# Kernel optimization log

Hardware: AMD Instinct MI355X
Metric: run time of the kernel (lower is better)

## Reference

```python
import jax, jax.numpy as jnp
import numpy as np

N, M, E, F, OUT = 20000, 2048, 320000, 512, 2
HID = F // 2
NEG_ATT = 0.2   # leaky_relu slope inside HypergraphConv attention
NEG = 0.01      # default F.leaky_relu / nn.LeakyReLU slope
EPS = 1e-5      # GraphNorm eps


def setup_inputs() -> dict:
    key = jax.random.key(0)
    ks = jax.random.split(key, 12)
    nrm = lambda k, shape, s=0.05: (jax.random.normal(k, shape, jnp.float32) * s)
    row = jax.random.randint(ks[1], (E,), 0, N)
    col = jax.random.randint(ks[2], (E,), 0, M)
    return dict(
        x=nrm(ks[0], (N, F), 1.0),
        edge_index=jnp.stack([row, col]),                 # [2, E] int32
        edge_attr=nrm(ks[3], (M, F), 1.0),
        W1=nrm(ks[4], (F, F)), att1=nrm(ks[5], (2 * F,)), b1=jnp.zeros((F,), jnp.float32),
        W2=nrm(ks[6], (F, F)), att2=nrm(ks[7], (2 * F,)), b2=jnp.zeros((F,), jnp.float32),
        gn1_w=jnp.ones((F,), jnp.float32), gn1_b=jnp.zeros((F,), jnp.float32), gn1_ms=jnp.ones((F,), jnp.float32),
        gn2_w=jnp.ones((F,), jnp.float32), gn2_b=jnp.zeros((F,), jnp.float32), gn2_ms=jnp.ones((F,), jnp.float32),
        fc1_W=nrm(ks[8], (F, HID)), fc1_b=jnp.zeros((HID,), jnp.float32),
        fc2_W=nrm(ks[9], (F, HID)), fc2_b=jnp.zeros((HID,), jnp.float32),
        cls_W=nrm(ks[10], (HID, OUT)), cls_b=jnp.zeros((OUT,), jnp.float32),
    )


def _segsum(v, idx, n):
    return jax.ops.segment_sum(v, idx, num_segments=n)


def hypergraph_conv(x, edge_attr, row, col, W, att, bias):
    """PyG HypergraphConv, heads=1, use_attention=True, attention_mode='node'."""
    xl = x @ W                          # [N, F] node features after lin
    el = edge_attr @ W                  # [M, F] hyperedge features after lin
    # attention logits per incidence: (cat[x_i, e_j] * att).sum(-1)
    pre = xl[row] @ att[:F] + el[col] @ att[F:]           # [E]
    alpha = jax.nn.leaky_relu(pre, NEG_ATT)
    # softmax grouped by hyperedge (col)
    amax = jax.ops.segment_max(alpha, col, num_segments=M)
    amax = jnp.where(jnp.isfinite(amax), amax, 0.0)
    ex = jnp.exp(alpha - amax[col])
    denom = _segsum(ex, col, M)
    alpha = ex / jnp.maximum(denom, 1e-16)[col]           # [E]
    # degree normalizations (hyperedge_weight = 1)
    ones = jnp.ones((row.shape[0],), xl.dtype)
    deg_n = _segsum(ones, row, N)
    Dinv = jnp.where(deg_n > 0, 1.0 / deg_n, 0.0)         # [N]
    deg_e = _segsum(ones, col, M)
    Binv = jnp.where(deg_e > 0, 1.0 / deg_e, 0.0)         # [M]
    # propagate 1: nodes -> hyperedges
    edge_feat = _segsum((alpha * Binv[col])[:, None] * xl[row], col, M)   # [M, F]
    # propagate 2: hyperedges -> nodes
    out = _segsum((alpha * Dinv[row])[:, None] * edge_feat[col], row, N)  # [N, F]
    return out + bias


def graph_norm(x, w, b, ms):
    # single graph (batch=None): normalize over all nodes
    mean = x.mean(axis=0)
    out = x - ms * mean
    var = (out * out).mean(axis=0)
    return out / jnp.sqrt(var + EPS) * w + b


def reference(x, edge_index, edge_attr,
              W1, att1, b1, W2, att2, b2,
              gn1_w, gn1_b, gn1_ms, gn2_w, gn2_b, gn2_ms,
              fc1_W, fc1_b, fc2_W, fc2_b, cls_W, cls_b):
    row, col = edge_index[0], edge_index[1]
    h = hypergraph_conv(x, edge_attr, row, col, W1, att1, b1)
    h = jax.nn.leaky_relu(graph_norm(h, gn1_w, gn1_b, gn1_ms), NEG)
    out = jax.nn.leaky_relu(h @ fc1_W + fc1_b, NEG)
    h = hypergraph_conv(h, edge_attr, row, col, W2, att2, b2)
    h = jax.nn.leaky_relu(graph_norm(h, gn2_w, gn2_b, gn2_ms), NEG)
    out = out + jax.nn.leaky_relu(h @ fc2_W + fc2_b, NEG)
    logits = out @ cls_W + cls_b
    return logits
```

## Files before the change

### kernel.cpp

```cpp
#include <hip/hip_runtime.h>
#include <math.h>

#define FDIM 512
#define HIDDIM 256
#define HB 128
#define SCH 1024
#define LDSK 32

typedef __bf16 bf16x8 __attribute__((ext_vector_type(8)));
typedef float floatx4 __attribute__((ext_vector_type(4)));

__device__ __forceinline__ float lrelu(float x, float s) { return x >= 0.0f ? x : s * x; }

__device__ __forceinline__ float bf2f(unsigned int u) {
  union { float f; unsigned int i; } v; v.i = u << 16; return v.f;
}
__device__ __forceinline__ unsigned short f2bf(float f) {
  union { float f; unsigned int u; } v; v.f = f;
  unsigned int x = v.u;
  return (unsigned short)((x + 0x7fffu + ((x >> 16) & 1u)) >> 16);
}

__device__ __forceinline__ void async_copy16(const unsigned short* g, unsigned short* l) {
  __builtin_amdgcn_global_load_lds((const __attribute__((address_space(1))) unsigned int*)g,
                                   (__attribute__((address_space(3))) unsigned int*)l, 16, 0, 0);
}

__device__ __forceinline__ float waveReduceSum(float v) {
#pragma unroll
  for (int o = 32; o; o >>= 1) v += __shfl_down(v, o, 64);
  return v;
}

__device__ __forceinline__ float blockReduceSum256(float v) {
  __shared__ float sm[4];
  int lane = threadIdx.x & 63, w = threadIdx.x >> 6;
  v = waveReduceSum(v);
  __syncthreads();
  if (lane == 0) sm[w] = v;
  __syncthreads();
  return sm[0] + sm[1] + sm[2] + sm[3];
}

__device__ __forceinline__ float blockReduceMax256(float v) {
  __shared__ float sm[4];
  int lane = threadIdx.x & 63, w = threadIdx.x >> 6;
#pragma unroll
  for (int o = 32; o; o >>= 1) v = fmaxf(v, __shfl_down(v, o, 64));
  __syncthreads();
  if (lane == 0) sm[w] = v;
  __syncthreads();
  return fmaxf(fmaxf(sm[0], sm[1]), fmaxf(sm[2], sm[3]));
}

__global__ __launch_bounds__(256) void k_hist2(const int* __restrict__ row, const int* __restrict__ col,
                                               int* __restrict__ cnt_r, int* __restrict__ cnt_c,
                                               int E, int nchunk) {
  __shared__ int h[2048];
  int b = blockIdx.x, t = threadIdx.x;
  for (int i = t; i < 2048; i += 256) h[i] = 0;
  __syncthreads();
  int s = b * nchunk, e = min(E, s + nchunk);
  for (int j = s + t; j < e; j += 256) {
    atomicAdd(&h[col[j]], 1);
    atomicAdd(&cnt_r[row[j]], 1);
  }
  __syncthreads();
  for (int i = t; i < 2048; i += 256) {
    int v = h[i];
    if (v) atomicAdd(&cnt_c[i], v);
  }
}

__global__ __launch_bounds__(256) void k_scan_part(const int* __restrict__ cnt, int* __restrict__ off,
                                                   int* __restrict__ btot, int n) {
  int b = blockIdx.x, t = threadIdx.x;
  int base = b * SCH + t * 4;
  int v[4];
#pragma unroll
  for (int i = 0; i < 4; ++i) v[i] = (base + i < n) ? cnt[base + i] : 0;
  int s = v[0] + v[1] + v[2] + v[3];
  int lane = t & 63, w = t >> 6;
  int x = s;
#pragma unroll
  for (int o = 1; o < 64; o <<= 1) {
    int y = __shfl_up(x, o, 64);
    if (lane >= o) x += y;
  }
  __shared__ int ws[4];
  if (lane == 63) ws[w] = x;
  __syncthreads();
  int wpre = 0;
  for (int i = 0; i < w; ++i) wpre += ws[i];
  int run = wpre + x - s;
#pragma unroll
  for (int i = 0; i < 4; ++i) {
    if (base + i < n) off[base + i] = run;
    run += v[i];
  }
  if (t == 255) btot[b] = wpre + x;
}

__global__ __launch_bounds__(256) void k_scan_midcol(int* __restrict__ btot, int nb,
                                                     const int* __restrict__ cnt_c, int* __restrict__ off_c,
                                                     int* __restrict__ gcur) {
  int t = threadIdx.x, lane = t & 63, w = t >> 6;
  __shared__ int ws[4];
  if (blockIdx.x == 0) {
    int v = (t < nb) ? btot[t] : 0;
    int x = v;
#pragma unroll
    for (int o = 1; o < 64; o <<= 1) {
      int y = __shfl_up(x, o, 64);
      if (lane >= o) x += y;
    }
    if (lane == 63) ws[w] = x;
    __syncthreads();
    int wpre = 0;
    for (int i = 0; i < w; ++i) wpre += ws[i];
    if (t < nb) btot[t] = wpre + x - v;
    if (t == 255) btot[nb] = wpre + x;
  } else {
    int base = t * 8;
    int v[8];
#pragma unroll
    for (int i = 0; i < 8; ++i) v[i] = cnt_c[base + i];
    int s = 0;
#pragma unroll
    for (int i = 0; i < 8; ++i) s += v[i];
    int x = s;
#pragma unroll
    for (int o = 1; o < 64; o <<= 1) {
      int y = __shfl_up(x, o, 64);
      if (lane >= o) x += y;
    }
    if (lane == 63) ws[w] = x;
    __syncthreads();
    int wpre = 0;
    for (int i = 0; i < w; ++i) wpre += ws[i];
    int run = wpre + x - s;
#pragma unroll
    for (int i = 0; i < 8; ++i) {
      off_c[base + i] = run;
      gcur[base + i] = run;
      run += v[i];
    }
    if (t == 255) off_c[2048] = wpre + x;
  }
}

__global__ __launch_bounds__(256) void k_scan_add(int* __restrict__ off, const int* __restrict__ btot,
                                                  int n, int nb) {
  int b = blockIdx.x, t = threadIdx.x;
  int base = b * SCH + t * 4;
  int add = btot[b];
#pragma unroll
  for (int i = 0; i < 4; ++i)
    if (base + i < n) off[base + i] += add;
  if (b == 0 && t == 0) off[n] = btot[nb];
}

__global__ __launch_bounds__(256) void k_fill3(const int* __restrict__ row, const int* __restrict__ col,
                                               int* __restrict__ gcur, const int* __restrict__ off_r,
                                               int* __restrict__ cur_r, int* __restrict__ csr_c,
                                               int* __restrict__ rj, int* __restrict__ cj,
                                               int* __restrict__ pos_r, int E, int nchunk) {
  __shared__ int h[2048];
  __shared__ int lbase[2048];
  int b = blockIdx.x, t = threadIdx.x;
  for (int i = t; i < 2048; i += 256) h[i] = 0;
  __syncthreads();
  int s = b * nchunk, e = min(E, s + nchunk);
  for (int j = s + t; j < e; j += 256) atomicAdd(&h[col[j]], 1);
  __syncthreads();
  for (int i = t; i < 2048; i += 256) {
    int c = h[i];
    lbase[i] = c ? atomicAdd(&gcur[i], c) : 0;
    h[i] = 0;
  }
  __syncthreads();
  for (int j = s + t; j < e; j += 256) {
    int r = row[j], c = col[j];
    int slot_c = lbase[c] + atomicAdd(&h[c], 1);
    csr_c[slot_c] = j;
    rj[slot_c] = r;
    int slot_r = off_r[r] + atomicAdd(&cur_r[r], 1);
    cj[slot_r] = c;
    pos_r[j] = slot_r;
  }
}

__global__ __launch_bounds__(256) void k_hi(const float* __restrict__ A, unsigned short* __restrict__ hi, int n4) {
  int i = blockIdx.x * 256 + threadIdx.x;
  if (i < n4) {
    float4 v = ((const float4*)A)[i];
    ushort4 h;
    h.x = f2bf(v.x); h.y = f2bf(v.y); h.z = f2bf(v.z); h.w = f2bf(v.w);
    ((ushort4*)hi)[i] = h;
  }
}

__global__ __launch_bounds__(256) void k_prep_w_hi2(const float* __restrict__ W1, unsigned short* __restrict__ t1,
                                                    const float* __restrict__ W2, unsigned short* __restrict__ t2,
                                                    int K, int Nc) {
  const float* W = blockIdx.z ? W2 : W1;
  unsigned short* th = blockIdx.z ? t2 : t1;
  int n = blockIdx.x * 16 + (threadIdx.x & 15);
  int k = blockIdx.y * 16 + (threadIdx.x >> 4);
  th[(size_t)n * K + k] = f2bf(W[(size_t)k * Nc + n]);
}

__global__ __launch_bounds__(256) void k_prep_w2(const float* __restrict__ Wa, unsigned short* __restrict__ tha,
                                                 unsigned short* __restrict__ tla, const float* __restrict__ Wb,
                                                 unsigned short* __restrict__ thb, unsigned short* __restrict__ tlb,
                                                 int K, int Nc) {
  const float* W = blockIdx.z ? Wb : Wa;
  unsigned short* th = blockIdx.z ? thb : tha;
  unsigned short* tl = blockIdx.z ? tlb : tla;
  int n = blockIdx.x * 16 + (threadIdx.x & 15);
  int k = blockIdx.y * 16 + (threadIdx.x >> 4);
  float v = W[(size_t)k * Nc + n];
  unsigned short h = f2bf(v);
  unsigned short l = f2bf(v - bf2f(h));
  th[(size_t)n * K + k] = h;
  tl[(size_t)n * K + k] = l;
}

__global__ __launch_bounds__(256) void k_wv2(const float* __restrict__ W1, const float* __restrict__ a1,
                                             const float* __restrict__ W2, const float* __restrict__ a2,
                                             float* __restrict__ wv1, float* __restrict__ wv2) {
  int lane = threadIdx.x & 63, w = threadIdx.x >> 6;
  int k = blockIdx.x * 4 + w;
  const float* W = blockIdx.y ? W2 : W1;
  const float* a = blockIdx.y ? a2 : a1;
  float* wv = blockIdx.y ? wv2 : wv1;
  float s = 0.f;
  for (int f = lane; f < FDIM; f += 64) s = fmaf(W[(size_t)k * FDIM + f], a[f], s);
  s = waveReduceSum(s);
  if (lane == 0) wv[k] = s;
}

__global__ __launch_bounds__(256) void k_ea2(const float* __restrict__ X, const float* __restrict__ wv1,
                                             const float* __restrict__ wv2, float* __restrict__ ea1,
                                             float* __restrict__ ea2, int Mr) {
  int lane = threadIdx.x & 63, w = threadIdx.x >> 6;
  int m = blockIdx.x * 4 + w;
  if (m < Mr) {
    float s1 = 0.f, s2 = 0.f;
    for (int f = lane; f < FDIM; f += 64) {
      float v = X[(size_t)m * FDIM + f];
      s1 = fmaf(v, wv1[f], s1);
      s2 = fmaf(v, wv2[f], s2);
    }
    s1 = waveReduceSum(s1);
    s2 = waveReduceSum(s2);
    if (lane == 0) { ea1[m] = s1; ea2[m] = s2; }
  }
}

__global__ __launch_bounds__(256, 1) void gemm_conv(const unsigned short* __restrict__ Ah,
                                                    const unsigned short* __restrict__ Bth,
                                                    unsigned short* __restrict__ Cb,
                                                    const float* __restrict__ att, float* __restrict__ xa,
                                                    int Mr, int K, int Nc) {
  __shared__ unsigned short lds[2 * 128 * LDSK];
  int tid = threadIdx.x, lane = tid & 63, w = tid >> 6;
  int wr = w >> 1, wc = w & 1;
  int rowB = blockIdx.y * 128, colB = blockIdx.x * 128;

  const unsigned short* src = (w < 2) ? Ah : Bth;
  int baseRow = ((w < 2) ? rowB : colB) + 64 * (w & 1);
  int maxRow = (w < 2) ? (Mr - 1) : (Nc - 1);
  int slr = lane >> 2, slc = lane & 3;
  unsigned short* dstBase = &lds[((w >> 1) * 128 + (w & 1) * 64) * LDSK];

  size_t gro[4];
#pragma unroll
  for (int seg = 0; seg < 4; ++seg) {
    int rg = baseRow + seg * 16 + slr;
    if (rg > maxRow) rg = maxRow;
    gro[seg] = (size_t)rg * K + slc * 8;
  }

  floatx4 zero4 = {0.f, 0.f, 0.f, 0.f};
  floatx4 acc[4][4];
#pragma unroll
  for (int i = 0; i < 4; ++i)
#pragma unroll
    for (int j = 0; j < 4; ++j) acc[i][j] = zero4;

  int fr = lane & 15, fq = lane >> 4;
  int offA = (wr * 64 + fr) * LDSK + fq * 8;
  int offB = 128 * LDSK + (wc * 64 + fr) * LDSK + fq * 8;

  for (int k0 = 0; k0 < K; k0 += 32) {
#pragma unroll
    for (int seg = 0; seg < 4; ++seg) async_copy16(src + gro[seg] + k0, dstBase + seg * 16 * LDSK);
    __syncthreads();
    bf16x8 a[4], b[4];
#pragma unroll
    for (int t = 0; t < 4; ++t) {
      a[t] = *(const bf16x8*)(&lds[offA + t * 16 * LDSK]);
      b[t] = *(const bf16x8*)(&lds[offB + t * 16 * LDSK]);
    }
#pragma unroll
    for (int ti = 0; ti < 4; ++ti)
#pragma unroll
      for (int tj = 0; tj < 4; ++tj)
        acc[ti][tj] = __builtin_amdgcn_mfma_f32_16x16x32_bf16(a[ti], b[tj], acc[ti][tj], 0, 0, 0);
    __syncthreads();
  }

  int colL = colB + wc * 64 + fr;
  int rowL = rowB + wr * 64 + fq * 4;
  float attv[4];
#pragma unroll
  for (int tj = 0; tj < 4; ++tj) attv[tj] = att[colL + tj * 16];
#pragma unroll
  for (int ti = 0; ti < 4; ++ti) {
#pragma unroll
    for (int r = 0; r < 4; ++r) {
      int rr = rowL + ti * 16 + r;
      if (rr < Mr) {
        float dot = 0.f;
#pragma unroll
        for (int tj = 0; tj < 4; ++tj) {
          float v = acc[ti][tj][r];
          Cb[(size_t)rr * Nc + colL + tj * 16] = f2bf(v);
          dot = fmaf(v, attv[tj], dot);
        }
#pragma unroll
        for (int o = 1; o < 16; o <<= 1) dot += __shfl_xor(dot, o, 64);
        if ((lane & 15) == 0) atomicAdd(&xa[rr], dot);
      }
    }
  }
}

template <int EPI>
__global__ __launch_bounds__(256, 1) void gemm_fc(const unsigned short* __restrict__ Ahi,
                                                  const unsigned short* __restrict__ Bthi,
                                                  const unsigned short* __restrict__ Btlo,
                                                  float* __restrict__ Cf, const float* __restrict__ bias,
                                                  int Mr, int K, int Nc) {
  __shared__ unsigned short lds[3 * 128 * LDSK];
  int tid = threadIdx.x, lane = tid & 63, w = tid >> 6;
  int wr = w >> 1, wc = w & 1;
  int rowB = blockIdx.y * 128, colB = blockIdx.x * 128;

  const unsigned short* src;
  int baseRow, maxRow, nseg;
  unsigned short* dstBase;
  if (w < 2) { src = Ahi; baseRow = rowB + 64 * w; maxRow = Mr - 1; nseg = 4; dstBase = &lds[w * 64 * LDSK]; }
  else if (w == 2) { src = Bthi; baseRow = colB; maxRow = Nc - 1; nseg = 8; dstBase = &lds[128 * LDSK]; }
  else { src = Btlo; baseRow = colB; maxRow = Nc - 1; nseg = 8; dstBase = &lds[2 * 128 * LDSK]; }

  int slr = lane >> 2, slc = lane & 3;
  size_t gro[8];
  for (int seg = 0; seg < nseg; ++seg) {
    int rg = baseRow + seg * 16 + slr;
    if (rg > maxRow) rg = maxRow;
    gro[seg] = (size_t)rg * K + slc * 8;
  }

  floatx4 zero4 = {0.f, 0.f, 0.f, 0.f};
  floatx4 acc[4][4];
#pragma unroll
  for (int i = 0; i < 4; ++i)
#pragma unroll
    for (int j = 0; j < 4; ++j) acc[i][j] = zero4;

  int fr = lane & 15, fq = lane >> 4;
  int offA = (wr * 64 + fr) * LDSK + fq * 8;
  int offBh = 128 * LDSK + (wc * 64 + fr) * LDSK + fq * 8;

  for (int k0 = 0; k0 < K; k0 += 32) {
    for (int seg = 0; seg < nseg; ++seg) async_copy16(src + gro[seg] + k0, dstBase + seg * 16 * LDSK);
    __syncthreads();
    bf16x8 a[4], bh[4], bl[4];
#pragma unroll
    for (int t = 0; t < 4; ++t) {
      a[t] = *(const bf16x8*)(&lds[offA + t * 16 * LDSK]);
      bh[t] = *(const bf16x8*)(&lds[offBh + t * 16 * LDSK]);
      bl[t] = *(const bf16x8*)(&lds[128 * LDSK + offBh + t * 16 * LDSK]);
    }
#pragma unroll
    for (int ti = 0; ti < 4; ++ti)
#pragma unroll
      for (int tj = 0; tj < 4; ++tj) {
        acc[ti][tj] = __builtin_amdgcn_mfma_f32_16x16x32_bf16(a[ti], bh[tj], acc[ti][tj], 0, 0, 0);
        acc[ti][tj] = __builtin_amdgcn_mfma_f32_16x16x32_bf16(a[ti], bl[tj], acc[ti][tj], 0, 0, 0);
      }
    __syncthreads();
  }

  int colL = colB + wc * 64 + fr;
  int rowL = rowB + wr * 64 + fq * 4;
#pragma unroll
  for (int tj = 0; tj < 4; ++tj) {
    int c = colL + tj * 16;
    float bb = bias[c];
#pragma unroll
    for (int ti = 0; ti < 4; ++ti) {
#pragma unroll
      for (int r = 0; r < 4; ++r) {
        int rr = rowL + ti * 16 + r;
        if (rr < Mr) {
          float v = lrelu(acc[ti][tj][r] + bb, 0.01f);
          if (EPI == 1) Cf[(size_t)rr * Nc + c] = v;
          else Cf[(size_t)rr * Nc + c] += v;
        }
      }
    }
  }
}

__global__ __launch_bounds__(256) void k_prop_col_f(const unsigned short* __restrict__ xl,
                                                    const float* __restrict__ xa, const float* __restrict__ ea,
                                                    const int* __restrict__ rj, const int* __restrict__ csr_c,
                                                    const int* __restrict__ pos_r, const int* __restrict__ off_c,
                                                    float* __restrict__ arj, unsigned short* __restrict__ ef) {
  int m = blockIdx.x;
  int s = off_c[m], e_ = off_c[m + 1];
  int cnt = e_ - s;
  float eam = ea[m];
  int t = threadIdx.x, lane = t & 63, w = t >> 6;

  float mx = -3.402823466e38f;
  for (int j = s + t; j < e_; j += 256) mx = fmaxf(mx, lrelu(xa[rj[j]] + eam, 0.2f));
  mx = blockReduceMax256(mx);
  float sum = 0.f;
  for (int j = s + t; j < e_; j += 256) sum += expf(lrelu(xa[rj[j]] + eam, 0.2f) - mx);
  sum = blockReduceSum256(sum);
  float inv = 1.0f / fmaxf(sum, 1e-16f);

  __shared__ int sidx[512];
  __shared__ float swgt[512];
  __shared__ float pf[4][512];
  float acc[8] = {0, 0, 0, 0, 0, 0, 0, 0};
  for (int base = 0; base < cnt; base += 512) {
    int n = min(512, cnt - base);
    for (int j = t; j < n; j += 256) {
      int g = s + base + j;
      int r = rj[g];
      float a = expf(lrelu(xa[r] + eam, 0.2f) - mx) * inv;
      sidx[j] = r;
      swgt[j] = a;
      arj[pos_r[csr_c[g]]] = a;
    }
    __syncthreads();
    int j = w;
    for (; j + 16 <= n; j += 16) {
      int r0 = sidx[j], r1 = sidx[j + 4], r2 = sidx[j + 8], r3 = sidx[j + 12];
      float w0 = swgt[j], w1 = swgt[j + 4], w2 = swgt[j + 8], w3 = swgt[j + 12];
      bf16x8 v0 = *(const bf16x8*)(xl + (size_t)r0 * FDIM + lane * 8);
      bf16x8 v1 = *(const bf16x8*)(xl + (size_t)r1 * FDIM + lane * 8);
      bf16x8 v2 = *(const bf16x8*)(xl + (size_t)r2 * FDIM + lane * 8);
      bf16x8 v3 = *(const bf16x8*)(xl + (size_t)r3 * FDIM + lane * 8);
#pragma unroll
      for (int i = 0; i < 8; ++i) acc[i] = fmaf(w0, (float)v0[i], acc[i]);
#pragma unroll
      for (int i = 0; i < 8; ++i) acc[i] = fmaf(w1, (float)v1[i], acc[i]);
#pragma unroll
      for (int i = 0; i < 8; ++i) acc[i] = fmaf(w2, (float)v2[i], acc[i]);
#pragma unroll
      for (int i = 0; i < 8; ++i) acc[i] = fmaf(w3, (float)v3[i], acc[i]);
    }
    for (; j < n; j += 4) {
      int r = sidx[j];
      float wt = swgt[j];
      bf16x8 v = *(const bf16x8*)(xl + (size_t)r * FDIM + lane * 8);
#pragma unroll
      for (int i = 0; i < 8; ++i) acc[i] = fmaf(wt, (float)v[i], acc[i]);
    }
    __syncthreads();
  }
  float binv = cnt > 0 ? 1.0f / (float)cnt : 0.0f;
#pragma unroll
  for (int i = 0; i < 8; i += 2) *(float2*)&pf[w][lane * 8 + i] = make_float2(acc[i] * binv, acc[i + 1] * binv);
  __syncthreads();
  float2 r0 = ((const float2*)pf[0])[t], r1 = ((const float2*)pf[1])[t];
  float2 r2 = ((const float2*)pf[2])[t], r3 = ((const float2*)pf[3])[t];
  float a0 = r0.x + r1.x + r2.x + r3.x;
  float a1 = r0.y + r1.y + r2.y + r3.y;
  unsigned int o = (unsigned int)f2bf(a0) | ((unsigned int)f2bf(a1) << 16);
  ((unsigned int*)(ef + (size_t)m * FDIM))[t] = o;
}

__global__ __launch_bounds__(256) void k_prop_row(const unsigned short* __restrict__ ef,
                                                  const float* __restrict__ arj, const int* __restrict__ cj,
                                                  const int* __restrict__ off_r, const float* __restrict__ bias,
                                                  unsigned short* __restrict__ hb) {
  int nB = blockIdx.x;
  int s = off_r[nB], e_ = off_r[nB + 1];
  int cnt = e_ - s;
  __shared__ int sidx[512];
  __shared__ float swgt[512];
  __shared__ float pf[4][512];
  int t = threadIdx.x, lane = t & 63, w = t >> 6;
  float acc[8] = {0, 0, 0, 0, 0, 0, 0, 0};
  for (int base = 0; base < cnt; base += 512) {
    int n = min(512, cnt - base);
    for (int j = t; j < n; j += 256) {
      sidx[j] = cj[s + base + j];
      swgt[j] = arj[s + base + j];
    }
    __syncthreads();
    int j = w;
    for (; j + 8 <= n; j += 8) {
      int r0 = sidx[j], r1 = sidx[j + 4];
      float w0 = swgt[j], w1 = swgt[j + 4];
      bf16x8 v0 = *(const bf16x8*)(ef + (size_t)r0 * FDIM + lane * 8);
      bf16x8 v1 = *(const bf16x8*)(ef + (size_t)r1 * FDIM + lane * 8);
#pragma unroll
      for (int i = 0; i < 8; ++i) acc[i] = fmaf(w0, (float)v0[i], acc[i]);
#pragma unroll
      for (int i = 0; i < 8; ++i) acc[i] = fmaf(w1, (float)v1[i], acc[i]);
    }
    for (; j < n; j += 4) {
      int r = sidx[j];
      float wt = swgt[j];
      bf16x8 v = *(const bf16x8*)(ef + (size_t)r * FDIM + lane * 8);
#pragma unroll
      for (int i = 0; i < 8; ++i) acc[i] = fmaf(wt, (float)v[i], acc[i]);
    }
    __syncthreads();
  }
  float dinv = cnt > 0 ? 1.0f / (float)cnt : 0.0f;
#pragma unroll
  for (int i = 0; i < 8; i += 2) *(float2*)&pf[w][lane * 8 + i] = make_float2(acc[i] * dinv, acc[i + 1] * dinv);
  __syncthreads();
  float2 r0 = ((const float2*)pf[0])[t], r1 = ((const float2*)pf[1])[t];
  float2 r2 = ((const float2*)pf[2])[t], r3 = ((const float2*)pf[3])[t];
  float a0 = r0.x + r1.x + r2.x + r3.x + bias[2 * t];
  float a1 = r0.y + r1.y + r2.y + r3.y + bias[2 * t + 1];
  unsigned int o = (unsigned int)f2bf(a0) | ((unsigned int)f2bf(a1) << 16);
  ((unsigned int*)(hb + (size_t)nB * FDIM))[t] = o;
}

__global__ __launch_bounds__(256) void k_stats(const unsigned short* __restrict__ hb, float* __restrict__ gsum,
                                               float* __restrict__ gsq, int N) {
  int t = threadIdx.x;
  float s0 = 0, q0 = 0, s1 = 0, q1 = 0;
  for (int r = blockIdx.x; r < N; r += gridDim.x) {
    unsigned int u = ((const unsigned int*)(hb + (size_t)r * FDIM))[t];
    float v0 = bf2f(u & 0xffffu), v1 = bf2f(u >> 16);
    s0 += v0; q0 = fmaf(v0, v0, q0);
    s1 += v1; q1 = fmaf(v1, v1, q1);
  }
  atomicAdd(&gsum[2 * t], s0);
  atomicAdd(&gsq[2 * t], q0);
  atomicAdd(&gsum[2 * t + 1], s1);
  atomicAdd(&gsq[2 * t + 1], q1);
}

__global__ __launch_bounds__(256) void k_napply(const unsigned short* __restrict__ hb,
                                                const float* __restrict__ gsum, const float* __restrict__ gsq,
                                                const float* __restrict__ ms, const float* __restrict__ wg,
                                                const float* __restrict__ b, unsigned short* __restrict__ hi,
                                                float invn, int total2) {
  int i = blockIdx.x * 256 + threadIdx.x;
  if (i < total2) {
    int f2 = i & 255;
    int f0 = 2 * f2, f1 = 2 * f2 + 1;
    float mean0 = gsum[f0] * invn, mean1 = gsum[f1] * invn;
    float m0 = ms[f0], m1 = ms[f1];
    float var0 = gsq[f0] * invn - (2.0f * m0 - m0 * m0) * mean0 * mean0;
    float var1 = gsq[f1] * invn - (2.0f * m1 - m1 * m1) * mean1 * mean1;
    float scl0 = wg[f0] * __frsqrt_rn(var0 + 1e-5f);
    float scl1 = wg[f1] * __frsqrt_rn(var1 + 1e-5f);
    unsigned int u = ((const unsigned int*)hb)[i];
    float v0 = bf2f(u & 0xffffu), v1 = bf2f(u >> 16);
    v0 = lrelu((v0 - m0 * mean0) * scl0 + b[f0], 0.01f);
    v1 = lrelu((v1 - m1 * mean1) * scl1 + b[f1], 0.01f);
    ((unsigned int*)hi)[i] = (unsigned int)f2bf(v0) | ((unsigned int)f2bf(v1) << 16);
  }
}

__global__ __launch_bounds__(256) void k_cls(const float* __restrict__ out1, const float* __restrict__ W,
                                             const float* __restrict__ b, float* __restrict__ logits, int N) {
  __shared__ float Ws[512];
  int t = threadIdx.x;
  Ws[t] = W[t];
  Ws[256 + t] = W[256 + t];
  __syncthreads();
  int lane = t & 63, w = t >> 6;
  int r = blockIdx.x * 4 + w;
  if (r < N) {
    float a0 = 0.f, a1 = 0.f;
    for (int k = lane; k < 256; k += 64) {
      float v = out1[(size_t)r * 256 + k];
      a0 = fmaf(v, Ws[2 * k], a0);
      a1 = fmaf(v, Ws[2 * k + 1], a1);
    }
#pragma unroll
    for (int o = 32; o; o >>= 1) {
      a0 += __shfl_down(a0, o, 64);
      a1 += __shfl_down(a1, o, 64);
    }
    if (lane == 0) {
      logits[(size_t)r * 2] = a0 + b[0];
      logits[(size_t)r * 2 + 1] = a1 + b[1];
    }
  }
}

extern "C" void kernel_launch(void* const* d_in, const int* in_sizes, int n_in,
                              void* d_out, int out_size, void* d_ws, size_t ws_size,
                              hipStream_t stream) {
  const float* x      = (const float*)d_in[0];
  const int*   eidx   = (const int*)d_in[1];
  const float* eattr  = (const float*)d_in[2];
  const float* W1     = (const float*)d_in[3];
  const float* att1   = (const float*)d_in[4];
  const float* b1     = (const float*)d_in[5];
  const float* W2     = (const float*)d_in[6];
  const float* att2   = (const float*)d_in[7];
  const float* b2     = (const float*)d_in[8];
  const float* gn1_w  = (const float*)d_in[9];
  const float* gn1_b  = (const float*)d_in[10];
  const float* gn1_ms = (const float*)d_in[11];
  const float* gn2_w  = (const float*)d_in[12];
  const float* gn2_b  = (const float*)d_in[13];
  const float* gn2_ms = (const float*)d_in[14];
  const float* fc1_W  = (const float*)d_in[15];
  const float* fc1_b  = (const float*)d_in[16];
  const float* fc2_W  = (const float*)d_in[17];
  const float* fc2_b  = (const float*)d_in[18];
  const float* cls_W  = (const float*)d_in[19];
  const float* cls_b  = (const float*)d_in[20];
  float* logits = (float*)d_out;

  const int N = in_sizes[0] / FDIM;
  const int E = in_sizes[1] / 2;
  const int M = in_sizes[2] / FDIM;
  const int* row = eidx;
  const int* col = eidx + E;
  const size_t NS = (size_t)N * FDIM;
  const size_t MS = (size_t)M * FDIM;

  char* base = (char*)d_ws;
  auto alloc = [&](size_t bytes) { char* r = base; base += (bytes + 255) & ~(size_t)255; return r; };

  unsigned short* xhi = (unsigned short*)alloc(NS * 2);
  unsigned short* xl  = (unsigned short*)alloc(NS * 2);
  unsigned short* hb  = (unsigned short*)alloc(NS * 2);
  unsigned short* ef  = (unsigned short*)alloc(MS * 2);
  float* out1 = (float*)alloc((size_t)N * HIDDIM * 4);
  unsigned short* w1th = (unsigned short*)alloc(FDIM * FDIM * 2);
  unsigned short* w2th = (unsigned short*)alloc(FDIM * FDIM * 2);
  unsigned short* f1th = (unsigned short*)alloc(FDIM * HIDDIM * 2);
  unsigned short* f1tl = (unsigned short*)alloc(FDIM * HIDDIM * 2);
  unsigned short* f2th = (unsigned short*)alloc(FDIM * HIDDIM * 2);
  unsigned short* f2tl = (unsigned short*)alloc(FDIM * HIDDIM * 2);
  float* wv1 = (float*)alloc(FDIM * 4);
  float* wv2 = (float*)alloc(FDIM * 4);
  float* ea1 = (float*)alloc((size_t)M * 4);
  float* ea2 = (float*)alloc((size_t)M * 4);
  float* arj = (float*)alloc((size_t)E * 4);
  int* off_r = (int*)alloc((size_t)(N + 1) * 4);
  int* off_c = (int*)alloc((size_t)(M + 1) * 4);
  int* gcur  = (int*)alloc((size_t)M * 4);
  int* csr_c = (int*)alloc((size_t)E * 4);
  int* rj    = (int*)alloc((size_t)E * 4);
  int* cj    = (int*)alloc((size_t)E * 4);
  int* pos_r = (int*)alloc((size_t)E * 4);
  int* btot  = (int*)alloc(512 * 4);

  char* zstart = base;
  int* cnt_r = (int*)alloc((size_t)(2 * N + M) * 4);
  int* cur_r = cnt_r + N;
  int* cnt_c = cur_r + N;
  float* xa1 = (float*)alloc((size_t)N * 4);
  float* xa2 = (float*)alloc((size_t)N * 4);
  float* gsum1 = (float*)alloc(FDIM * 4);
  float* gsq1  = (float*)alloc(FDIM * 4);
  float* gsum2 = (float*)alloc(FDIM * 4);
  float* gsq2  = (float*)alloc(FDIM * 4);
  size_t zlen = (size_t)(base - zstart);
  hipMemsetAsync(zstart, 0, zlen, stream);

  int nchunk = (E + HB - 1) / HB;
  int nbR = (N + SCH - 1) / SCH;
  k_hist2<<<HB, 256, 0, stream>>>(row, col, cnt_r, cnt_c, E, nchunk);
  k_scan_part<<<nbR, 256, 0, stream>>>(cnt_r, off_r, btot, N);
  k_scan_midcol<<<2, 256, 0, stream>>>(btot, nbR, cnt_c, off_c, gcur);
  k_scan_add<<<nbR, 256, 0, stream>>>(off_r, btot, N, nbR);
  k_fill3<<<HB, 256, 0, stream>>>(row, col, gcur, off_r, cur_r, csr_c, rj, cj, pos_r, E, nchunk);

  k_hi<<<(int)((NS / 4 + 255) / 256), 256, 0, stream>>>(x, xhi, (int)(NS / 4));
  k_prep_w_hi2<<<dim3(FDIM / 16, FDIM / 16, 2), 256, 0, stream>>>(W1, w1th, W2, w2th, FDIM, FDIM);
  k_prep_w2<<<dim3(HIDDIM / 16, FDIM / 16, 2), 256, 0, stream>>>(fc1_W, f1th, f1tl, fc2_W, f2th, f2tl, FDIM, HIDDIM);
  k_wv2<<<dim3(FDIM / 4, 2), 256, 0, stream>>>(W1, att1 + FDIM, W2, att2 + FDIM, wv1, wv2);
  k_ea2<<<(M + 3) / 4, 256, 0, stream>>>(eattr, wv1, wv2, ea1, ea2, M);

  int gN128 = (N + 127) / 128;
  int napply_grid = (int)((NS / 2 + 255) / 256);
  float invn = 1.0f / (float)N;

  gemm_conv<<<dim3(FDIM / 128, gN128), 256, 0, stream>>>(xhi, w1th, xl, att1, xa1, N, FDIM, FDIM);
  k_prop_col_f<<<M, 256, 0, stream>>>(xl, xa1, ea1, rj, csr_c, pos_r, off_c, arj, ef);
  k_prop_row<<<N, 256, 0, stream>>>(ef, arj, cj, off_r, b1, hb);
  k_stats<<<256, 256, 0, stream>>>(hb, gsum1, gsq1, N);
  k_napply<<<napply_grid, 256, 0, stream>>>(hb, gsum1, gsq1, gn1_ms, gn1_w, gn1_b, xhi, invn, (int)(NS / 2));
  gemm_fc<1><<<dim3(HIDDIM / 128, gN128), 256, 0, stream>>>(xhi, f1th, f1tl, out1, fc1_b, N, FDIM, HIDDIM);

  gemm_conv<<<dim3(FDIM / 128, gN128), 256, 0, stream>>>(xhi, w2th, xl, att2, xa2, N, FDIM, FDIM);
  k_prop_col_f<<<M, 256, 0, stream>>>(xl, xa2, ea2, rj, csr_c, pos_r, off_c, arj, ef);
  k_prop_row<<<N, 256, 0, stream>>>(ef, arj, cj, off_r, b2, hb);
  k_stats<<<256, 256, 0, stream>>>(hb, gsum2, gsq2, N);
  k_napply<<<napply_grid, 256, 0, stream>>>(hb, gsum2, gsq2, gn2_ms, gn2_w, gn2_b, xhi, invn, (int)(NS / 2));
  gemm_fc<2><<<dim3(HIDDIM / 128, gN128), 256, 0, stream>>>(xhi, f2th, f2tl, out1, fc2_b, N, FDIM, HIDDIM);

  k_cls<<<(N + 3) / 4, 256, 0, stream>>>(out1, cls_W, cls_b, logits, N);
}
```

Before: 579.5 us.

## Fuse both FC GEMMs with classifier and cache softmax logits in LDS

Merges the two fc GEMMs and the classifier into one kernel. Each block computes both fc tiles for a 64-column slice, applies bias and leaky-relu, and atomically adds its partial logits, so the fp32 out1 buffer and the separate k_cls pass go away. The normalized activations of each layer now go to separate buffers. Hyperedge softmax now stores logits in LDS when degree is at most 512, avoiding repeated gathers of xa. The csr_c/pos_r double indirection becomes a single prj array. The trade-offs are more atomics on logits, nondeterministic summation order, and two extra activation buffers.

```diff
diff --git a/kernel.cpp b/kernel.cpp
--- a/kernel.cpp
+++ b/kernel.cpp
@@ -162,9 +162,9 @@
 
 __global__ __launch_bounds__(256) void k_fill3(const int* __restrict__ row, const int* __restrict__ col,
                                                int* __restrict__ gcur, const int* __restrict__ off_r,
-                                               int* __restrict__ cur_r, int* __restrict__ csr_c,
+                                               int* __restrict__ cur_r, int* __restrict__ prj,
                                                int* __restrict__ rj, int* __restrict__ cj,
-                                               int* __restrict__ pos_r, int E, int nchunk) {
+                                               int E, int nchunk) {
   __shared__ int h[2048];
   __shared__ int lbase[2048];
   int b = blockIdx.x, t = threadIdx.x;
@@ -182,11 +182,10 @@
   for (int j = s + t; j < e; j += 256) {
     int r = row[j], c = col[j];
     int slot_c = lbase[c] + atomicAdd(&h[c], 1);
-    csr_c[slot_c] = j;
+    int slot_r = off_r[r] + atomicAdd(&cur_r[r], 1);
     rj[slot_c] = r;
-    int slot_r = off_r[r] + atomicAdd(&cur_r[r], 1);
+    prj[slot_c] = slot_r;
     cj[slot_r] = c;
-    pos_r[j] = slot_r;
   }
 }
 
@@ -337,78 +336,120 @@
   }
 }
 
-template <int EPI>
-__global__ __launch_bounds__(256, 1) void gemm_fc(const unsigned short* __restrict__ Ahi,
-                                                  const unsigned short* __restrict__ Bthi,
-                                                  const unsigned short* __restrict__ Btlo,
-                                                  float* __restrict__ Cf, const float* __restrict__ bias,
-                                                  int Mr, int K, int Nc) {
-  __shared__ unsigned short lds[3 * 128 * LDSK];
+__global__ __launch_bounds__(256, 1) void gemm_fc_cls(const unsigned short* __restrict__ A1,
+                                                      const unsigned short* __restrict__ B1h,
+                                                      const unsigned short* __restrict__ B1l,
+                                                      const float* __restrict__ b1,
+                                                      const unsigned short* __restrict__ A2,
+                                                      const unsigned short* __restrict__ B2h,
+                                                      const unsigned short* __restrict__ B2l,
+                                                      const float* __restrict__ b2,
+                                                      const float* __restrict__ clsW, const float* __restrict__ clsb,
+                                                      float* __restrict__ logits, int Mr, int K) {
+  __shared__ unsigned short lds[(128 + 2 * 64) * LDSK];
   int tid = threadIdx.x, lane = tid & 63, w = tid >> 6;
   int wr = w >> 1, wc = w & 1;
-  int rowB = blockIdx.y * 128, colB = blockIdx.x * 128;
-
-  const unsigned short* src;
-  int baseRow, maxRow, nseg;
-  unsigned short* dstBase;
-  if (w < 2) { src = Ahi; baseRow = rowB + 64 * w; maxRow = Mr - 1; nseg = 4; dstBase = &lds[w * 64 * LDSK]; }
-  else if (w == 2) { src = Bthi; baseRow = colB; maxRow = Nc - 1; nseg = 8; dstBase = &lds[128 * LDSK]; }
-  else { src = Btlo; baseRow = colB; maxRow = Nc - 1; nseg = 8; dstBase = &lds[2 * 128 * LDSK]; }
+  int rowB = blockIdx.y * 128, colB = blockIdx.x * 64;
 
   int slr = lane >> 2, slc = lane & 3;
-  size_t gro[8];
-  for (int seg = 0; seg < nseg; ++seg) {
+  int baseRow = (w < 2) ? (rowB + 64 * w) : colB;
+  int maxRow = (w < 2) ? (Mr - 1) : (HIDDIM - 1);
+  unsigned short* dstBase = &lds[w * 64 * LDSK];
+
+  size_t gro[4];
+#pragma unroll
+  for (int seg = 0; seg < 4; ++seg) {
     int rg = baseRow + seg * 16 + slr;
     if (rg > maxRow) rg = maxRow;
     gro[seg] = (size_t)rg * K + slc * 8;
   }
 
-  floatx4 zero4 = {0.f, 0.f, 0.f, 0.f};
-  floatx4 acc[4][4];
-#pragma unroll
-  for (int i = 0; i < 4; ++i)
-#pragma unroll
-    for (int j = 0; j < 4; ++j) acc[i][j] = zero4;
-
   int fr = lane & 15, fq = lane >> 4;
   int offA = (wr * 64 + fr) * LDSK + fq * 8;
-  int offBh = 128 * LDSK + (wc * 64 + fr) * LDSK + fq * 8;
-
-  for (int k0 = 0; k0 < K; k0 += 32) {
-    for (int seg = 0; seg < nseg; ++seg) async_copy16(src + gro[seg] + k0, dstBase + seg * 16 * LDSK);
-    __syncthreads();
-    bf16x8 a[4], bh[4], bl[4];
-#pragma unroll
-    for (int t = 0; t < 4; ++t) {
-      a[t] = *(const bf16x8*)(&lds[offA + t * 16 * LDSK]);
-      bh[t] = *(const bf16x8*)(&lds[offBh + t * 16 * LDSK]);
-      bl[t] = *(const bf16x8*)(&lds[128 * LDSK + offBh + t * 16 * LDSK]);
-    }
-#pragma unroll
-    for (int ti = 0; ti < 4; ++ti)
-#pragma unroll
-      for (int tj = 0; tj < 4; ++tj) {
-        acc[ti][tj] = __builtin_amdgcn_mfma_f32_16x16x32_bf16(a[ti], bh[tj], acc[ti][tj], 0, 0, 0);
-        acc[ti][tj] = __builtin_amdgcn_mfma_f32_16x16x32_bf16(a[ti], bl[tj], acc[ti][tj], 0, 0, 0);
+  int offBh = (128 + wc * 32 + fr) * LDSK + fq * 8;
+  int offBl = offBh + 64 * LDSK;
+
+  floatx4 zero4 = {0.f, 0.f, 0.f, 0.f};
+  floatx4 acc1[4][2], acc2[4][2];
+#pragma unroll
+  for (int i = 0; i < 4; ++i) {
+    acc1[i][0] = zero4; acc1[i][1] = zero4;
+    acc2[i][0] = zero4; acc2[i][1] = zero4;
+  }
+
+#pragma unroll
+  for (int L = 0; L < 2; ++L) {
+    const unsigned short* src =
+        (L == 0) ? ((w < 2) ? A1 : (w == 2) ? B1h : B1l)
+                 : ((w < 2) ? A2 : (w == 2) ? B2h : B2l);
+    for (int k0 = 0; k0 < K; k0 += 32) {
+#pragma unroll
+      for (int seg = 0; seg < 4; ++seg) async_copy16(src + gro[seg] + k0, dstBase + seg * 16 * LDSK);
+      __syncthreads();
+      bf16x8 a[4], bh[2], bl[2];
+#pragma unroll
+      for (int t = 0; t < 4; ++t) a[t] = *(const bf16x8*)(&lds[offA + t * 16 * LDSK]);
+#pragma unroll
+      for (int t = 0; t < 2; ++t) {
+        bh[t] = *(const bf16x8*)(&lds[offBh + t * 16 * LDSK]);
+        bl[t] = *(const bf16x8*)(&lds[offBl + t * 16 * LDSK]);
       }
-    __syncthreads();
-  }
-
-  int colL = colB + wc * 64 + fr;
+      if (L == 0) {
+#pragma unroll
+        for (int ti = 0; ti < 4; ++ti)
+#pragma unroll
+          for (int tj = 0; tj < 2; ++tj) {
+            acc1[ti][tj] = __builtin_amdgcn_mfma_f32_16x16x32_bf16(a[ti], bh[tj], acc1[ti][tj], 0, 0, 0);
+            acc1[ti][tj] = __builtin_amdgcn_mfma_f32_16x16x32_bf16(a[ti], bl[tj], acc1[ti][tj], 0, 0, 0);
+          }
+      } else {
+#pragma unroll
+        for (int ti = 0; ti < 4; ++ti)
+#pragma unroll
+          for (int tj = 0; tj < 2; ++tj) {
+            acc2[ti][tj] = __builtin_amdgcn_mfma_f32_16x16x32_bf16(a[ti], bh[tj], acc2[ti][tj], 0, 0, 0);
+            acc2[ti][tj] = __builtin_amdgcn_mfma_f32_16x16x32_bf16(a[ti], bl[tj], acc2[ti][tj], 0, 0, 0);
+          }
+      }
+      __syncthreads();
+    }
+  }
+
+  int colL = colB + wc * 32 + fr;
   int rowL = rowB + wr * 64 + fq * 4;
-#pragma unroll
-  for (int tj = 0; tj < 4; ++tj) {
+  float cw0[2], cw1[2], bb1[2], bb2[2];
+#pragma unroll
+  for (int tj = 0; tj < 2; ++tj) {
     int c = colL + tj * 16;
-    float bb = bias[c];
-#pragma unroll
-    for (int ti = 0; ti < 4; ++ti) {
-#pragma unroll
-      for (int r = 0; r < 4; ++r) {
-        int rr = rowL + ti * 16 + r;
-        if (rr < Mr) {
-          float v = lrelu(acc[ti][tj][r] + bb, 0.01f);
-          if (EPI == 1) Cf[(size_t)rr * Nc + c] = v;
-          else Cf[(size_t)rr * Nc + c] += v;
+    cw0[tj] = clsW[2 * c];
+    cw1[tj] = clsW[2 * c + 1];
+    bb1[tj] = b1[c];
+    bb2[tj] = b2[c];
+  }
+  bool addBias = (blockIdx.x == 0 && wc == 0);
+  float cb0 = clsb[0], cb1 = clsb[1];
+#pragma unroll
+  for (int ti = 0; ti < 4; ++ti) {
+#pragma unroll
+    for (int r = 0; r < 4; ++r) {
+      int rr = rowL + ti * 16 + r;
+      if (rr < Mr) {
+        float d0 = 0.f, d1 = 0.f;
+#pragma unroll
+        for (int tj = 0; tj < 2; ++tj) {
+          float v = lrelu(acc1[ti][tj][r] + bb1[tj], 0.01f) + lrelu(acc2[ti][tj][r] + bb2[tj], 0.01f);
+          d0 = fmaf(v, cw0[tj], d0);
+          d1 = fmaf(v, cw1[tj], d1);
+        }
+#pragma unroll
+        for (int o = 1; o < 16; o <<= 1) {
+          d0 += __shfl_xor(d0, o, 64);
+          d1 += __shfl_xor(d1, o, 64);
+        }
+        if ((lane & 15) == 0) {
+          if (addBias) { d0 += cb0; d1 += cb1; }
+          atomicAdd(&logits[2 * (size_t)rr], d0);
+          atomicAdd(&logits[2 * (size_t)rr + 1], d1);
         }
       }
     }
@@ -417,8 +458,8 @@
 
 __global__ __launch_bounds__(256) void k_prop_col_f(const unsigned short* __restrict__ xl,
                                                     const float* __restrict__ xa, const float* __restrict__ ea,
-                                                    const int* __restrict__ rj, const int* __restrict__ csr_c,
-                                                    const int* __restrict__ pos_r, const int* __restrict__ off_c,
+                                                    const int* __restrict__ rj, const int* __restrict__ prj,
+                                                    const int* __restrict__ off_c,
                                                     float* __restrict__ arj, unsigned short* __restrict__ ef) {
   int m = blockIdx.x;
   int s = off_c[m], e_ = off_c[m + 1];
@@ -426,31 +467,33 @@
   float eam = ea[m];
   int t = threadIdx.x, lane = t & 63, w = t >> 6;
 
-  float mx = -3.402823466e38f;
-  for (int j = s + t; j < e_; j += 256) mx = fmaxf(mx, lrelu(xa[rj[j]] + eam, 0.2f));
-  mx = blockReduceMax256(mx);
-  float sum = 0.f;
-  for (int j = s + t; j < e_; j += 256) sum += expf(lrelu(xa[rj[j]] + eam, 0.2f) - mx);
-  sum = blockReduceSum256(sum);
-  float inv = 1.0f / fmaxf(sum, 1e-16f);
-
   __shared__ int sidx[512];
   __shared__ float swgt[512];
   __shared__ float pf[4][512];
   float acc[8] = {0, 0, 0, 0, 0, 0, 0, 0};
-  for (int base = 0; base < cnt; base += 512) {
-    int n = min(512, cnt - base);
-    for (int j = t; j < n; j += 256) {
-      int g = s + base + j;
-      int r = rj[g];
-      float a = expf(lrelu(xa[r] + eam, 0.2f) - mx) * inv;
+
+  if (cnt <= 512) {
+    float mx = -3.402823466e38f;
+    for (int j = t; j < cnt; j += 256) {
+      int r = rj[s + j];
+      float lg = lrelu(xa[r] + eam, 0.2f);
       sidx[j] = r;
+      swgt[j] = lg;
+      mx = fmaxf(mx, lg);
+    }
+    mx = blockReduceMax256(mx);
+    float sum = 0.f;
+    for (int j = t; j < cnt; j += 256) sum += expf(swgt[j] - mx);
+    sum = blockReduceSum256(sum);
+    float inv = 1.0f / fmaxf(sum, 1e-16f);
+    for (int j = t; j < cnt; j += 256) {
+      float a = expf(swgt[j] - mx) * inv;
       swgt[j] = a;
-      arj[pos_r[csr_c[g]]] = a;
+      arj[prj[s + j]] = a;
     }
     __syncthreads();
     int j = w;
-    for (; j + 16 <= n; j += 16) {
+    for (; j + 16 <= cnt; j += 16) {
       int r0 = sidx[j], r1 = sidx[j + 4], r2 = sidx[j + 8], r3 = sidx[j + 12];
       float w0 = swgt[j], w1 = swgt[j + 4], w2 = swgt[j + 8], w3 = swgt[j + 12];
       bf16x8 v0 = *(const bf16x8*)(xl + (size_t)r0 * FDIM + lane * 8);
@@ -466,7 +509,7 @@
 #pragma unroll
       for (int i = 0; i < 8; ++i) acc[i] = fmaf(w3, (float)v3[i], acc[i]);
     }
-    for (; j < n; j += 4) {
+    for (; j < cnt; j += 4) {
       int r = sidx[j];
       float wt = swgt[j];
       bf16x8 v = *(const bf16x8*)(xl + (size_t)r * FDIM + lane * 8);
@@ -474,7 +517,44 @@
       for (int i = 0; i < 8; ++i) acc[i] = fmaf(wt, (float)v[i], acc[i]);
     }
     __syncthreads();
-  }
+  } else {
+    float mx = -3.402823466e38f;
+    for (int j = s + t; j < e_; j += 256) mx = fmaxf(mx, lrelu(xa[rj[j]] + eam, 0.2f));
+    mx = blockReduceMax256(mx);
+    float sum = 0.f;
+    for (int j = s + t; j < e_; j += 256) sum += expf(lrelu(xa[rj[j]] + eam, 0.2f) - mx);
+    sum = blockReduceSum256(sum);
+    float inv = 1.0f / fmaxf(sum, 1e-16f);
+    for (int base = 0; base < cnt; base += 512) {
+      int n = min(512, cnt - base);
+      for (int j = t; j < n; j += 256) {
+        int g = s + base + j;
+        int r = rj[g];
+        float a = expf(lrelu(xa[r] + eam, 0.2f) - mx) * inv;
+        sidx[j] = r;
+        swgt[j] = a;
+        arj[prj[g]] = a;
+      }
+      __syncthreads();
+      int j = w;
+      for (; j + 4 <= n; j += 4) {
+        int r = sidx[j];
+        float wt = swgt[j];
+        bf16x8 v = *(const bf16x8*)(xl + (size_t)r * FDIM + lane * 8);
+#pragma unroll
+        for (int i = 0; i < 8; ++i) acc[i] = fmaf(wt, (float)v[i], acc[i]);
+      }
+      if (j < n) {
+        int r = sidx[j];
+        float wt = swgt[j];
+        bf16x8 v = *(const bf16x8*)(xl + (size_t)r * FDIM + lane * 8);
+#pragma unroll
+        for (int i = 0; i < 8; ++i) acc[i] = fmaf(wt, (float)v[i], acc[i]);
+      }
+      __syncthreads();
+    }
+  }
+
   float binv = cnt > 0 ? 1.0f / (float)cnt : 0.0f;
 #pragma unroll
   for (int i = 0; i < 8; i += 2) *(float2*)&pf[w][lane * 8 + i] = make_float2(acc[i] * binv, acc[i + 1] * binv);
@@ -574,34 +654,6 @@
     v0 = lrelu((v0 - m0 * mean0) * scl0 + b[f0], 0.01f);
     v1 = lrelu((v1 - m1 * mean1) * scl1 + b[f1], 0.01f);
     ((unsigned int*)hi)[i] = (unsigned int)f2bf(v0) | ((unsigned int)f2bf(v1) << 16);
-  }
-}
-
-__global__ __launch_bounds__(256) void k_cls(const float* __restrict__ out1, const float* __restrict__ W,
-                                             const float* __restrict__ b, float* __restrict__ logits, int N) {
-  __shared__ float Ws[512];
-  int t = threadIdx.x;
-  Ws[t] = W[t];
-  Ws[256 + t] = W[256 + t];
-  __syncthreads();
-  int lane = t & 63, w = t >> 6;
-  int r = blockIdx.x * 4 + w;
-  if (r < N) {
-    float a0 = 0.f, a1 = 0.f;
-    for (int k = lane; k < 256; k += 64) {
-      float v = out1[(size_t)r * 256 + k];
-      a0 = fmaf(v, Ws[2 * k], a0);
-      a1 = fmaf(v, Ws[2 * k + 1], a1);
-    }
-#pragma unroll
-    for (int o = 32; o; o >>= 1) {
-      a0 += __shfl_down(a0, o, 64);
-      a1 += __shfl_down(a1, o, 64);
-    }
-    if (lane == 0) {
-      logits[(size_t)r * 2] = a0 + b[0];
-      logits[(size_t)r * 2 + 1] = a1 + b[1];
-    }
   }
 }
 
@@ -643,10 +695,11 @@
   auto alloc = [&](size_t bytes) { char* r = base; base += (bytes + 255) & ~(size_t)255; return r; };
 
   unsigned short* xhi = (unsigned short*)alloc(NS * 2);
+  unsigned short* xh1 = (unsigned short*)alloc(NS * 2);
+  unsigned short* xh2 = (unsigned short*)alloc(NS * 2);
   unsigned short* xl  = (unsigned short*)alloc(NS * 2);
   unsigned short* hb  = (unsigned short*)alloc(NS * 2);
   unsigned short* ef  = (unsigned short*)alloc(MS * 2);
-  float* out1 = (float*)alloc((size_t)N * HIDDIM * 4);
   unsigned short* w1th = (unsigned short*)alloc(FDIM * FDIM * 2);
   unsigned short* w2th = (unsigned short*)alloc(FDIM * FDIM * 2);
   unsigned short* f1th = (unsigned short*)alloc(FDIM * HIDDIM * 2);
@@ -661,10 +714,9 @@
   int* off_r = (int*)alloc((size_t)(N + 1) * 4);
   int* off_c = (int*)alloc((size_t)(M + 1) * 4);
   int* gcur  = (int*)alloc((size_t)M * 4);
-  int* csr_c = (int*)alloc((size_t)E * 4);
   int* rj    = (int*)alloc((size_t)E * 4);
   int* cj    = (int*)alloc((size_t)E * 4);
-  int* pos_r = (int*)alloc((size_t)E * 4);
+  int* prj   = (int*)alloc((size_t)E * 4);
   int* btot  = (int*)alloc(512 * 4);
 
   char* zstart = base;
@@ -679,6 +731,7 @@
   float* gsq2  = (float*)alloc(FDIM * 4);
   size_t zlen = (size_t)(base - zstart);
   hipMemsetAsync(zstart, 0, zlen, stream);
+  hipMemsetAsync(logits, 0, (size_t)N * 2 * sizeof(float), stream);
 
   int nchunk = (E + HB - 1) / HB;
   int nbR = (N + SCH - 1) / SCH;
@@ -686,7 +739,7 @@
   k_scan_part<<<nbR, 256, 0, stream>>>(cnt_r, off_r, btot, N);
   k_scan_midcol<<<2, 256, 0, stream>>>(btot, nbR, cnt_c, off_c, gcur);
   k_scan_add<<<nbR, 256, 0, stream>>>(off_r, btot, N, nbR);
-  k_fill3<<<HB, 256, 0, stream>>>(row, col, gcur, off_r, cur_r, csr_c, rj, cj, pos_r, E, nchunk);
+  k_fill3<<<HB, 256, 0, stream>>>(row, col, gcur, off_r, cur_r, prj, rj, cj, E, nchunk);
 
   k_hi<<<(int)((NS / 4 + 255) / 256), 256, 0, stream>>>(x, xhi, (int)(NS / 4));
   k_prep_w_hi2<<<dim3(FDIM / 16, FDIM / 16, 2), 256, 0, stream>>>(W1, w1th, W2, w2th, FDIM, FDIM);
@@ -699,18 +752,18 @@
   float invn = 1.0f / (float)N;
 
   gemm_conv<<<dim3(FDIM / 128, gN128), 256, 0, stream>>>(xhi, w1th, xl, att1, xa1, N, FDIM, FDIM);
-  k_prop_col_f<<<M, 256, 0, stream>>>(xl, xa1, ea1, rj, csr_c, pos_r, off_c, arj, ef);
+  k_prop_col_f<<<M, 256, 0, stream>>>(xl, xa1, ea1, rj, prj, off_c, arj, ef);
   k_prop_row<<<N, 256, 0, stream>>>(ef, arj, cj, off_r, b1, hb);
   k_stats<<<256, 256, 0, stream>>>(hb, gsum1, gsq1, N);
-  k_napply<<<napply_grid, 256, 0, stream>>>(hb, gsum1, gsq1, gn1_ms, gn1_w, gn1_b, xhi, invn, (int)(NS / 2));
-  gemm_fc<1><<<dim3(HIDDIM / 128, gN128), 256, 0, stream>>>(xhi, f1th, f1tl, out1, fc1_b, N, FDIM, HIDDIM);
-
-  gemm_conv<<<dim3(FDIM / 128, gN128), 256, 0, stream>>>(xhi, w2th, xl, att2, xa2, N, FDIM, FDIM);
-  k_prop_col_f<<<M, 256, 0, stream>>>(xl, xa2, ea2, rj, csr_c, pos_r, off_c, arj, ef);
+  k_napply<<<napply_grid, 256, 0, stream>>>(hb, gsum1, gsq1, gn1_ms, gn1_w, gn1_b, xh1, invn, (int)(NS / 2));
+
+  gemm_conv<<<dim3(FDIM / 128, gN128), 256, 0, stream>>>(xh1, w2th, xl, att2, xa2, N, FDIM, FDIM);
+  k_prop_col_f<<<M, 256, 0, stream>>>(xl, xa2, ea2, rj, prj, off_c, arj, ef);
   k_prop_row<<<N, 256, 0, stream>>>(ef, arj, cj, off_r, b2, hb);
   k_stats<<<256, 256, 0, stream>>>(hb, gsum2, gsq2, N);
-  k_napply<<<napply_grid, 256, 0, stream>>>(hb, gsum2, gsq2, gn2_ms, gn2_w, gn2_b, xhi, invn, (int)(NS / 2));
-  gemm_fc<2><<<dim3(HIDDIM / 128, gN128), 256, 0, stream>>>(xhi, f2th, f2tl, out1, fc2_b, N, FDIM, HIDDIM);
-
-  k_cls<<<(N + 3) / 4, 256, 0, stream>>>(out1, cls_W, cls_b, logits, N);
-}
+  k_napply<<<napply_grid, 256, 0, stream>>>(hb, gsum2, gsq2, gn2_ms, gn2_w, gn2_b, xh2, invn, (int)(NS / 2));
+
+  gemm_fc_cls<<<dim3(HIDDIM / 64, gN128), 256, 0, stream>>>(xh1, f1th, f1tl, fc1_b,
+                                                            xh2, f2th, f2tl, fc2_b,
+                                                            cls_W, cls_b, logits, N, FDIM);
+}
```

New measurement: 540.0 us. 1.07x faster.
